# Optimization experiments

Measured on AMD Instinct MI355X. Metric: run time of the kernel, lower is better.

Reference implementation:

```python
import jax, jax.numpy as jnp
import numpy as np

EPS = 1.1920929e-07  # torch fp32 finfo eps used by F.rms_norm default

def rms_norm(x):
    return x * jax.lax.rsqrt(jnp.mean(jnp.square(x), axis=-1, keepdims=True) + EPS)

def setup_inputs() -> dict:
    key = jax.random.key(0)
    kx, kfc, kpr, krt = jax.random.split(key, 4)
    B, T, C, F = 4, 2048, 2048, 8192
    s = (3.0 ** 0.5) * C ** -0.5  # init scale used in init_weights
    x = jax.random.normal(kx, (B, T, C), dtype=jnp.float32)
    w_fc = jax.random.normal(kfc, (F, C), dtype=jnp.float32) * s
    w_proj = jax.random.normal(kpr, (C, F), dtype=jnp.float32) * (s * 0.1)
    w_router = jax.random.normal(krt, (1, C), dtype=jnp.float32) * 0.01  # router init std=0.01
    return {"x": x, "w_fc": w_fc, "w_proj": w_proj, "w_router": w_router}

def reference(x, w_fc, w_proj, w_router):
    # Router: (B,T,C) @ (C,1) -> (B,T) logits; STE mask (~0 or ~1 floats)
    logits = jnp.einsum('btc,oc->bto', x, w_router)[..., 0]  # (B,T)
    prob = jax.nn.sigmoid(logits)
    hard = (prob > 0.5).astype(x.dtype)
    mask_i = hard + prob - jax.lax.stop_gradient(prob)  # straight-through
    mask_bool = mask_i > 0.5  # (B,T)

    # Gated MLP (mixture-of-depth). The torch code gathers selected tokens,
    # runs the MLP on the compacted set, scatters into zeros, and multiplies
    # by mask_i. Mathematically identical dense form (honoring the mask):
    h = jnp.einsum('btc,fc->btf', rms_norm(x), w_fc)
    h = jnp.square(jax.nn.relu(h))  # relu(x)^2 activation
    mlp_out = jnp.einsum('btf,cf->btc', h, w_proj)
    gated = jnp.where(mask_bool[..., None], mlp_out * mask_i[..., None], 0.0)
    return x + gated
```

## Files before the change

kernel.cpp:

```cpp
#include <hip/hip_runtime.h>
#include <type_traits>
#include <utility>
#include <stdint.h>
#include <stddef.h>

#define TOKENS 8192
#define CDIM 2048
#define FDIM 8192
#define EPSV 1.1920929e-07f

typedef __attribute__((ext_vector_type(8))) short short8;
typedef __attribute__((ext_vector_type(8))) __bf16 bf16x8;
typedef __attribute__((ext_vector_type(4))) float floatx4;

template <typename V, typename = void> struct CanMfma : std::false_type {};
template <typename V>
struct CanMfma<V, std::void_t<decltype(__builtin_amdgcn_mfma_f32_16x16x32_bf16(
    std::declval<V>(), std::declval<V>(), std::declval<floatx4>(), 0, 0, 0))>>
    : std::true_type {};
using frag_t = std::conditional_t<CanMfma<short8>::value, short8, bf16x8>;

__device__ __forceinline__ floatx4 mfma_bf16(frag_t a, frag_t b, floatx4 c) {
    return __builtin_amdgcn_mfma_f32_16x16x32_bf16(a, b, c, 0, 0, 0);
}

__device__ __forceinline__ unsigned short f2bf(float f) {
    unsigned int u = __float_as_uint(f);
    u += 0x7fffu + ((u >> 16) & 1u);
    return (unsigned short)(u >> 16);
}

__global__ void zero_kernel(int* p) { if (threadIdx.x == 0) *p = 0; }

__global__ __launch_bounds__(256) void cvt_kernel(const float* __restrict__ src,
                                                  unsigned short* __restrict__ dst, int n4) {
    int i = blockIdx.x * 256 + threadIdx.x;
    if (i < n4) {
        float4 v = ((const float4*)src)[i];
        ushort4 o;
        o.x = f2bf(v.x); o.y = f2bf(v.y); o.z = f2bf(v.z); o.w = f2bf(v.w);
        ((ushort4*)dst)[i] = o;
    }
}

__global__ __launch_bounds__(256) void router_kernel(
    const float* __restrict__ x, const float* __restrict__ wr,
    float* __restrict__ out, unsigned short* __restrict__ Xn,
    int* __restrict__ idx, float* __restrict__ mv, int* __restrict__ cnt)
{
    const int token = blockIdx.x;
    const int tid = threadIdx.x;
    const float4* xr = (const float4*)(x + (size_t)token * CDIM);
    const float4* w4 = (const float4*)wr;
    float4 a0 = xr[tid];
    float4 a1 = xr[tid + 256];
    float4 b0 = w4[tid];
    float4 b1 = w4[tid + 256];
    float ss = a0.x*a0.x + a0.y*a0.y + a0.z*a0.z + a0.w*a0.w
             + a1.x*a1.x + a1.y*a1.y + a1.z*a1.z + a1.w*a1.w;
    float dt = a0.x*b0.x + a0.y*b0.y + a0.z*b0.z + a0.w*b0.w
             + a1.x*b1.x + a1.y*b1.y + a1.z*b1.z + a1.w*b1.w;
    #pragma unroll
    for (int off = 32; off > 0; off >>= 1) {
        ss += __shfl_down(ss, off);
        dt += __shfl_down(dt, off);
    }
    __shared__ float red_ss[4], red_dt[4];
    __shared__ float s_rms;
    __shared__ int s_pos;
    const int wave = tid >> 6;
    if ((tid & 63) == 0) { red_ss[wave] = ss; red_dt[wave] = dt; }
    __syncthreads();
    if (tid == 0) {
        float S = red_ss[0] + red_ss[1] + red_ss[2] + red_ss[3];
        float D = red_dt[0] + red_dt[1] + red_dt[2] + red_dt[3];
        float prob = 1.0f / (1.0f + expf(-D));
        s_rms = 1.0f / sqrtf(S * (1.0f / (float)CDIM) + EPSV);
        int pos = -1;
        if (prob > 0.5f) {
            pos = atomicAdd(cnt, 1);
            idx[pos] = token;
            mv[pos] = (1.0f + prob) - prob;
        }
        s_pos = pos;
    }
    __syncthreads();
    const float rms = s_rms;
    const int pos = s_pos;
    if (pos >= 0) {
        ushort4* xp = (ushort4*)(Xn + (size_t)pos * CDIM);
        ushort4 o;
        o.x = f2bf(a0.x * rms); o.y = f2bf(a0.y * rms); o.z = f2bf(a0.z * rms); o.w = f2bf(a0.w * rms);
        xp[tid] = o;
        o.x = f2bf(a1.x * rms); o.y = f2bf(a1.y * rms); o.z = f2bf(a1.z * rms); o.w = f2bf(a1.w * rms);
        xp[tid + 256] = o;
    } else {
        float4* op = (float4*)(out + (size_t)token * CDIM);
        op[tid] = a0;
        op[tid + 256] = a1;
    }
}

template <int K, int MODE, int LDO>
__global__ __launch_bounds__(256) void gemm_bt(
    const unsigned short* __restrict__ A,
    const unsigned short* __restrict__ B,
    unsigned short* __restrict__ Hout,
    float* __restrict__ out,
    const float* __restrict__ xres,
    const int* __restrict__ idx,
    const float* __restrict__ mv,
    const int* __restrict__ cntp)
{
    const int cnt = *cntp;
    const int m0 = blockIdx.x * 128;
    if (m0 >= cnt) return;
    const int n0 = blockIdx.y * 128;

    __shared__ alignas(16) unsigned short lA[128 * 64];
    __shared__ alignas(16) unsigned short lB[128 * 64];

    const int tid = threadIdx.x;
    const int wave = tid >> 6;
    const int lane = tid & 63;
    const int wm = (wave >> 1) * 64;
    const int wn = (wave & 1) * 64;
    const int quad = lane >> 4;
    const int l16 = lane & 15;

    const int srow = lane >> 3;
    const int schunk = (lane & 7) ^ srow;

    const unsigned short* ap[4];
    const unsigned short* bp[4];
    #pragma unroll
    for (int p = 0; p < 4; ++p) {
        const int r = p * 32 + wave * 8 + srow;
        ap[p] = A + (size_t)(m0 + r) * K + schunk * 8;
        bp[p] = B + (size_t)(n0 + r) * K + schunk * 8;
    }

    floatx4 acc[4][4] = {};

    for (int kt = 0; kt < K / 64; ++kt) {
        #pragma unroll
        for (int p = 0; p < 4; ++p) {
            __builtin_amdgcn_global_load_lds(
                (__attribute__((address_space(1))) void*)ap[p],
                (__attribute__((address_space(3))) void*)&lA[(p * 32 + wave * 8) * 64],
                16, 0, 0);
            __builtin_amdgcn_global_load_lds(
                (__attribute__((address_space(1))) void*)bp[p],
                (__attribute__((address_space(3))) void*)&lB[(p * 32 + wave * 8) * 64],
                16, 0, 0);
            ap[p] += 64;
            bp[p] += 64;
        }
        __syncthreads();
        #pragma unroll
        for (int s = 0; s < 2; ++s) {
            frag_t af[4], bfv[4];
            #pragma unroll
            for (int t = 0; t < 4; ++t) {
                const int ra = wm + t * 16 + l16;
                const int ca = ((s * 4 + quad) ^ (ra & 7)) * 8;
                af[t] = *(const frag_t*)&lA[ra * 64 + ca];
                const int rb = wn + t * 16 + l16;
                const int cb = ((s * 4 + quad) ^ (rb & 7)) * 8;
                bfv[t] = *(const frag_t*)&lB[rb * 64 + cb];
            }
            #pragma unroll
            for (int tm = 0; tm < 4; ++tm)
                #pragma unroll
                for (int tn = 0; tn < 4; ++tn)
                    acc[tm][tn] = mfma_bf16(af[tm], bfv[tn], acc[tm][tn]);
        }
        __syncthreads();
    }

    if (MODE == 1) {
        #pragma unroll
        for (int tm = 0; tm < 4; ++tm) {
            const int gm = m0 + wm + tm * 16 + quad * 4;
            #pragma unroll
            for (int tn = 0; tn < 4; ++tn) {
                const int gn = n0 + wn + tn * 16 + l16;
                #pragma unroll
                for (int v = 0; v < 4; ++v) {
                    float h = fmaxf(acc[tm][tn][v], 0.0f);
                    Hout[(size_t)(gm + v) * LDO + gn] = f2bf(h * h);
                }
            }
        }
    } else {
        #pragma unroll
        for (int tm = 0; tm < 4; ++tm) {
            const int gmb = m0 + wm + tm * 16 + quad * 4;
            #pragma unroll
            for (int v = 0; v < 4; ++v) {
                const int gm = gmb + v;
                if (gm < cnt) {
                    const int token = idx[gm];
                    const float scale = mv[gm];
                    #pragma unroll
                    for (int tn = 0; tn < 4; ++tn) {
                        const int gn = n0 + wn + tn * 16 + l16;
                        const size_t o = (size_t)token * LDO + gn;
                        out[o] = xres[o] + scale * acc[tm][tn][v];
                    }
                }
            }
        }
    }
}

extern "C" void kernel_launch(void* const* d_in, const int* in_sizes, int n_in,
                              void* d_out, int out_size, void* d_ws, size_t ws_size,
                              hipStream_t stream)
{
    const float* x   = (const float*)d_in[0];
    const float* wfc = (const float*)d_in[1];
    const float* wpr = (const float*)d_in[2];
    const float* wrt = (const float*)d_in[3];
    float* out = (float*)d_out;

    char* ws = (char*)d_ws;
    int*   cnt = (int*)ws;
    int*   idx = (int*)(ws + 256);
    float* mv  = (float*)(ws + 256 + 32768);
    unsigned short* Xn  = (unsigned short*)(ws + 65792);
    unsigned short* Wfc = (unsigned short*)(ws + 65792 + 33554432ULL);
    unsigned short* Wpr = (unsigned short*)(ws + 65792 + 67108864ULL);
    unsigned short* H   = (unsigned short*)(ws + 65792 + 100663296ULL);

    zero_kernel<<<1, 64, 0, stream>>>(cnt);
    cvt_kernel<<<(FDIM * CDIM / 4) / 256, 256, 0, stream>>>(wfc, Wfc, FDIM * CDIM / 4);
    cvt_kernel<<<(CDIM * FDIM / 4) / 256, 256, 0, stream>>>(wpr, Wpr, CDIM * FDIM / 4);
    router_kernel<<<TOKENS, 256, 0, stream>>>(x, wrt, out, Xn, idx, mv, cnt);
    gemm_bt<CDIM, 1, FDIM><<<dim3(TOKENS / 128, FDIM / 128), 256, 0, stream>>>(
        Xn, Wfc, H, nullptr, nullptr, nullptr, nullptr, cnt);
    gemm_bt<FDIM, 2, CDIM><<<dim3(TOKENS / 128, CDIM / 128), 256, 0, stream>>>(
        H, Wpr, nullptr, out, x, idx, mv, cnt);
}
```

Measured before the change: 815.9 us.

## Split-K second GEMM with atomic accumulation, swizzle block order, fuse weight conversions

The second GEMM is split along K into two halves. Each half atomically adds its scaled partial result into the output, and the router now pre-writes x into out for every token, so the residual read is no longer needed. Both GEMMs remap block indices into 8x8 groups to improve L2 reuse of A and B tiles. The two weight-conversion launches are merged into one kernel. Split-K doubles the grid for the narrow C-dimension GEMM to fill more CUs, at the cost of float atomics, an extra full write of out, and nondeterministic summation order.

```diff
diff --git a/kernel.cpp b/kernel.cpp
--- a/kernel.cpp
+++ b/kernel.cpp
@@ -32,15 +32,19 @@
 
 __global__ void zero_kernel(int* p) { if (threadIdx.x == 0) *p = 0; }
 
-__global__ __launch_bounds__(256) void cvt_kernel(const float* __restrict__ src,
-                                                  unsigned short* __restrict__ dst, int n4) {
+__global__ __launch_bounds__(256) void cvt2_kernel(
+    const float* __restrict__ s1, unsigned short* __restrict__ d1, int n1,
+    const float* __restrict__ s2, unsigned short* __restrict__ d2, int n2)
+{
     int i = blockIdx.x * 256 + threadIdx.x;
-    if (i < n4) {
-        float4 v = ((const float4*)src)[i];
-        ushort4 o;
-        o.x = f2bf(v.x); o.y = f2bf(v.y); o.z = f2bf(v.z); o.w = f2bf(v.w);
-        ((ushort4*)dst)[i] = o;
-    }
+    const float4* s; ushort4* d;
+    if (i < n1) { s = (const float4*)s1; d = (ushort4*)d1; }
+    else if (i < n1 + n2) { s = (const float4*)s2; d = (ushort4*)d2; i -= n1; }
+    else return;
+    float4 v = s[i];
+    ushort4 o;
+    o.x = f2bf(v.x); o.y = f2bf(v.y); o.z = f2bf(v.z); o.w = f2bf(v.w);
+    d[i] = o;
 }
 
 __global__ __launch_bounds__(256) void router_kernel(
@@ -85,6 +89,9 @@
         s_pos = pos;
     }
     __syncthreads();
+    float4* op = (float4*)(out + (size_t)token * CDIM);
+    op[tid] = a0;
+    op[tid + 256] = a1;
     const float rms = s_rms;
     const int pos = s_pos;
     if (pos >= 0) {
@@ -94,28 +101,29 @@
         xp[tid] = o;
         o.x = f2bf(a1.x * rms); o.y = f2bf(a1.y * rms); o.z = f2bf(a1.z * rms); o.w = f2bf(a1.w * rms);
         xp[tid + 256] = o;
-    } else {
-        float4* op = (float4*)(out + (size_t)token * CDIM);
-        op[tid] = a0;
-        op[tid + 256] = a1;
-    }
-}
-
-template <int K, int MODE, int LDO>
+    }
+}
+
+template <int K, int MODE, int LDO, int KSPLIT>
 __global__ __launch_bounds__(256) void gemm_bt(
     const unsigned short* __restrict__ A,
     const unsigned short* __restrict__ B,
     unsigned short* __restrict__ Hout,
     float* __restrict__ out,
-    const float* __restrict__ xres,
     const int* __restrict__ idx,
     const float* __restrict__ mv,
     const int* __restrict__ cntp)
 {
     const int cnt = *cntp;
-    const int m0 = blockIdx.x * 128;
+    const int bid = blockIdx.y * 64 + blockIdx.x;
+    const int s = bid >> 6;
+    const int w = bid & 63;
+    const int mi = (s & 7) * 8 + (w & 7);
+    const int ni = (s >> 3) * 8 + (w >> 3);
+    const int m0 = mi * 128;
     if (m0 >= cnt) return;
-    const int n0 = blockIdx.y * 128;
+    const int n0 = ni * 128;
+    const int k0 = (int)blockIdx.z * (K / KSPLIT);
 
     __shared__ alignas(16) unsigned short lA[128 * 64];
     __shared__ alignas(16) unsigned short lB[128 * 64];
@@ -136,13 +144,13 @@
     #pragma unroll
     for (int p = 0; p < 4; ++p) {
         const int r = p * 32 + wave * 8 + srow;
-        ap[p] = A + (size_t)(m0 + r) * K + schunk * 8;
-        bp[p] = B + (size_t)(n0 + r) * K + schunk * 8;
+        ap[p] = A + (size_t)(m0 + r) * K + k0 + schunk * 8;
+        bp[p] = B + (size_t)(n0 + r) * K + k0 + schunk * 8;
     }
 
     floatx4 acc[4][4] = {};
 
-    for (int kt = 0; kt < K / 64; ++kt) {
+    for (int kt = 0; kt < K / (64 * KSPLIT); ++kt) {
         #pragma unroll
         for (int p = 0; p < 4; ++p) {
             __builtin_amdgcn_global_load_lds(
@@ -158,15 +166,15 @@
         }
         __syncthreads();
         #pragma unroll
-        for (int s = 0; s < 2; ++s) {
+        for (int st = 0; st < 2; ++st) {
             frag_t af[4], bfv[4];
             #pragma unroll
             for (int t = 0; t < 4; ++t) {
                 const int ra = wm + t * 16 + l16;
-                const int ca = ((s * 4 + quad) ^ (ra & 7)) * 8;
+                const int ca = ((st * 4 + quad) ^ (ra & 7)) * 8;
                 af[t] = *(const frag_t*)&lA[ra * 64 + ca];
                 const int rb = wn + t * 16 + l16;
-                const int cb = ((s * 4 + quad) ^ (rb & 7)) * 8;
+                const int cb = ((st * 4 + quad) ^ (rb & 7)) * 8;
                 bfv[t] = *(const frag_t*)&lB[rb * 64 + cb];
             }
             #pragma unroll
@@ -205,8 +213,7 @@
                     #pragma unroll
                     for (int tn = 0; tn < 4; ++tn) {
                         const int gn = n0 + wn + tn * 16 + l16;
-                        const size_t o = (size_t)token * LDO + gn;
-                        out[o] = xres[o] + scale * acc[tm][tn][v];
+                        atomicAdd(&out[(size_t)token * LDO + gn], scale * acc[tm][tn][v]);
                     }
                 }
             }
@@ -233,12 +240,12 @@
     unsigned short* Wpr = (unsigned short*)(ws + 65792 + 67108864ULL);
     unsigned short* H   = (unsigned short*)(ws + 65792 + 100663296ULL);
 
+    const int n4 = FDIM * CDIM / 4;
     zero_kernel<<<1, 64, 0, stream>>>(cnt);
-    cvt_kernel<<<(FDIM * CDIM / 4) / 256, 256, 0, stream>>>(wfc, Wfc, FDIM * CDIM / 4);
-    cvt_kernel<<<(CDIM * FDIM / 4) / 256, 256, 0, stream>>>(wpr, Wpr, CDIM * FDIM / 4);
+    cvt2_kernel<<<(2 * n4 + 255) / 256, 256, 0, stream>>>(wfc, Wfc, n4, wpr, Wpr, n4);
     router_kernel<<<TOKENS, 256, 0, stream>>>(x, wrt, out, Xn, idx, mv, cnt);
-    gemm_bt<CDIM, 1, FDIM><<<dim3(TOKENS / 128, FDIM / 128), 256, 0, stream>>>(
-        Xn, Wfc, H, nullptr, nullptr, nullptr, nullptr, cnt);
-    gemm_bt<FDIM, 2, CDIM><<<dim3(TOKENS / 128, CDIM / 128), 256, 0, stream>>>(
-        H, Wpr, nullptr, out, x, idx, mv, cnt);
-}
+    gemm_bt<CDIM, 1, FDIM, 1><<<dim3(64, FDIM / 128), 256, 0, stream>>>(
+        Xn, Wfc, H, nullptr, nullptr, nullptr, cnt);
+    gemm_bt<FDIM, 2, CDIM, 2><<<dim3(64, CDIM / 128, 2), 256, 0, stream>>>(
+        H, Wpr, nullptr, out, idx, mv, cnt);
+}
```

Measured after the change: 704.9 us. 1.16x faster.
